# Optimization experiments

Hardware: AMD Instinct MI355X
Metric: run time of the kernel (lower is better)

Reference implementation:

```python
import jax, jax.numpy as jnp
import numpy as np

B, T, C, H = 32, 500, 256, 8  # batch, seq, n_embd(=in_c), heads


def setup_inputs() -> dict:
    key = jax.random.key(0)
    ks = jax.random.split(key, 6)
    s = 0.02
    return {
        "x": jax.random.normal(ks[0], (B, T, C), dtype=jnp.float32),
        # nn.Linear(in_c, 3*n_embd): store as [in, out] for x @ W
        "W_attn": jax.random.normal(ks[1], (C, 3 * C), dtype=jnp.float32) * s,
        "b_attn": jnp.zeros((3 * C,), dtype=jnp.float32),
        # nn.Conv1d(heads, 1, 1, bias=False): a per-head mixing weight [H]
        "p_w": jax.random.normal(ks[2], (H,), dtype=jnp.float32) * s,
        # nn.Linear(n_embd, n_embd)
        "W_proj": jax.random.normal(ks[3], (C, C), dtype=jnp.float32) * s,
        "b_proj": jnp.zeros((C,), dtype=jnp.float32),
    }


def reference(x, W_attn, b_attn, p_w, W_proj, b_proj):
    Bx, Tx, Cx = x.shape
    Hh = p_w.shape[0]
    d = Cx // Hh
    qkv = x @ W_attn + b_attn                          # [B,T,3C]
    q, k, v = jnp.split(qkv, 3, axis=-1)
    # [B,T,C] -> [B,H,T,d]
    q = q.reshape(Bx, Tx, Hh, d).transpose(0, 2, 1, 3)
    k = k.reshape(Bx, Tx, Hh, d).transpose(0, 2, 1, 3)
    v = v.reshape(Bx, Tx, Hh, d).transpose(0, 2, 1, 3)
    scale = 1.0 / np.sqrt(d).astype(np.float32)
    att = jnp.einsum('bhtd,bhsd->bhts', q, k) * scale  # [B,H,T,T]
    # bias buffer is all ones for T<=500, so masked_fill is a no-op
    # pred path: 1x1 conv over heads (weighted sum), then sigmoid
    pred_weight = jax.nn.sigmoid(jnp.einsum('bhts,h->bts', att, p_w))  # [B,T,T]
    pred_weight = jnp.where(jnp.isnan(pred_weight), 0.0, pred_weight)
    # value path: softmax @ V
    a = jax.nn.softmax(att, axis=-1)                   # [B,H,T,T]
    ctx = jnp.einsum('bhts,bhsd->bhtd', a, v)          # [B,H,T,d]
    ctx = ctx.transpose(0, 2, 1, 3).reshape(Bx, Tx, Cx)  # [B,T,C]
    value = ctx @ W_proj + b_proj
    return (pred_weight, value)
```

## Files before the change

### kernel.cpp

```cpp
#include <hip/hip_runtime.h>
#include <stddef.h>

typedef unsigned short u16;
typedef unsigned int u32;
typedef __attribute__((ext_vector_type(4))) float f32x4;
typedef __attribute__((ext_vector_type(8))) u16 u16x8;
typedef __attribute__((ext_vector_type(8))) short s16x8;
typedef __attribute__((ext_vector_type(4))) u32 u32x4;

#define MFMA16 __builtin_amdgcn_mfma_f32_16x16x32_bf16

__device__ __forceinline__ float bf2f(u16 u) { return __uint_as_float(((u32)u) << 16); }
__device__ __forceinline__ u16 f2bf(float f) {
  u32 u = __float_as_uint(f);
  return (u16)((u + 0x7FFFu + ((u >> 16) & 1u)) >> 16);
}
__device__ __forceinline__ u32 cvt_pk_bf16(float lo, float hi) {
  u32 r; asm("v_cvt_pk_bf16_f32 %0, %1, %2" : "=v"(r) : "v"(lo), "v"(hi)); return r;
}

union frag_u { u32x4 u; s16x8 s; };


__global__ __launch_bounds__(256) void gemm_qkv(
    const float* __restrict__ x, const float* __restrict__ W,
    const float* __restrict__ bias, u16* __restrict__ qkbuf, u16* __restrict__ vt)
{
  __shared__ u16 As[128][32];
  __shared__ u16 Bs[64][40];
  const int tid = threadIdx.x;
  const int lane = tid & 63;
  const int w = tid >> 6;
  const int cl = lane & 15, g = lane >> 4;
  const int m0 = blockIdx.x * 128, n0 = blockIdx.y * 64;
  const int wm = w >> 1, wn = w & 1;
  const int bn = tid & 63, bk8 = (tid >> 6) * 8;
  const int ar0 = tid >> 2, ac0 = (tid & 3) * 8;
  const int ar1 = (tid + 256) >> 2, ac1 = ((tid + 256) & 3) * 8;

  f32x4 acc[4][2];
#pragma unroll
  for (int mi = 0; mi < 4; ++mi)
#pragma unroll
    for (int ni = 0; ni < 2; ++ni) acc[mi][ni] = (f32x4){0.f, 0.f, 0.f, 0.f};

  for (int kt = 0; kt < 8; ++kt) {
    const int k0 = kt * 32;
    f32x4 a0l = *(const f32x4*)&x[(size_t)(m0 + ar0) * 256 + k0 + ac0];
    f32x4 a0h = *(const f32x4*)&x[(size_t)(m0 + ar0) * 256 + k0 + ac0 + 4];
    f32x4 a1l = *(const f32x4*)&x[(size_t)(m0 + ar1) * 256 + k0 + ac1];
    f32x4 a1h = *(const f32x4*)&x[(size_t)(m0 + ar1) * 256 + k0 + ac1 + 4];
    float wv[8];
#pragma unroll
    for (int j = 0; j < 8; ++j)
      wv[j] = W[(size_t)(k0 + bk8 + j) * 768 + n0 + bn];
    __syncthreads();
    u32x4 p0, p1;
    p0[0] = cvt_pk_bf16(a0l[0], a0l[1]); p0[1] = cvt_pk_bf16(a0l[2], a0l[3]);
    p0[2] = cvt_pk_bf16(a0h[0], a0h[1]); p0[3] = cvt_pk_bf16(a0h[2], a0h[3]);
    p1[0] = cvt_pk_bf16(a1l[0], a1l[1]); p1[1] = cvt_pk_bf16(a1l[2], a1l[3]);
    p1[2] = cvt_pk_bf16(a1h[0], a1h[1]); p1[3] = cvt_pk_bf16(a1h[2], a1h[3]);
    *(u32x4*)&As[ar0][ac0] = p0;
    *(u32x4*)&As[ar1][ac1] = p1;
    u32x4 bw;
    bw[0] = cvt_pk_bf16(wv[0], wv[1]); bw[1] = cvt_pk_bf16(wv[2], wv[3]);
    bw[2] = cvt_pk_bf16(wv[4], wv[5]); bw[3] = cvt_pk_bf16(wv[6], wv[7]);
    *(u32x4*)&Bs[bn][bk8] = bw;
    __syncthreads();
    s16x8 af[4], bfr[2];
#pragma unroll
    for (int mi = 0; mi < 4; ++mi) af[mi] = *(const s16x8*)&As[wm * 64 + mi * 16 + cl][g * 8];
#pragma unroll
    for (int ni = 0; ni < 2; ++ni) bfr[ni] = *(const s16x8*)&Bs[wn * 32 + ni * 16 + cl][g * 8];
#pragma unroll
    for (int mi = 0; mi < 4; ++mi)
#pragma unroll
      for (int ni = 0; ni < 2; ++ni)
        acc[mi][ni] = MFMA16(af[mi], bfr[ni], acc[mi][ni], 0, 0, 0);
  }
  float bb[2] = { bias[n0 + wn * 32 + cl], bias[n0 + wn * 32 + 16 + cl] };
  if (n0 < 512) {
#pragma unroll
    for (int mi = 0; mi < 4; ++mi)
#pragma unroll
      for (int ni = 0; ni < 2; ++ni)
#pragma unroll
        for (int r = 0; r < 4; ++r) {
          int m = m0 + wm * 64 + mi * 16 + g * 4 + r;
          qkbuf[(size_t)m * 512 + n0 + wn * 32 + ni * 16 + cl] = f2bf(acc[mi][ni][r] + bb[ni]);
        }
  } else {
#pragma unroll
    for (int mi = 0; mi < 4; ++mi)
#pragma unroll
      for (int ni = 0; ni < 2; ++ni) {
        int cb = n0 - 512 + wn * 32 + ni * 16 + cl;
#pragma unroll
        for (int r = 0; r < 4; ++r) {
          int m = m0 + wm * 64 + mi * 16 + g * 4 + r;
          int b2 = m / 500;
          int t2 = m - b2 * 500;
          vt[(size_t)(b2 * 256 + cb) * 500 + t2] = f2bf(acc[mi][ni][r] + bb[ni]);
        }
      }
  }
}

__global__ __launch_bounds__(256) void pred_gemm(
    const u16* __restrict__ qk, const float* __restrict__ pw_g,
    float* __restrict__ pred)
{
  const int tid = threadIdx.x;
  const int lane = tid & 63;
  const int w = tid >> 6;
  const int cl = lane & 15, g = lane >> 4;
  const int lin = blockIdx.x;
  const int xcd = lin & 7, idx = lin >> 3;
  const int b = xcd * 4 + (idx >> 4);
  const int tile = idx & 15;
  const int tm = tile >> 2, tn = tile & 3;
  const int r0 = tm * 128 + (w >> 1) * 64;
  const int c0 = tn * 128 + (w & 1) * 64;
  const float scale = 0.17677669529663687f;

  const u16* qkb = qk + (size_t)b * 500 * 512;
  float fw[8];
#pragma unroll
  for (int h = 0; h < 8; ++h) fw[h] = pw_g[h] * scale;

  f32x4 acc[4][4];
#pragma unroll
  for (int mi = 0; mi < 4; ++mi)
#pragma unroll
    for (int ni = 0; ni < 4; ++ni) acc[mi][ni] = (f32x4){0.f, 0.f, 0.f, 0.f};

#pragma unroll 2
  for (int kt = 0; kt < 8; ++kt) {
    const int k0 = kt * 32;
    s16x8 af[4], bf[4];
#pragma unroll
    for (int mi = 0; mi < 4; ++mi) {
      int t = r0 + mi * 16 + cl; if (t > 499) t = 499;
      af[mi] = *(const s16x8*)&qkb[(size_t)t * 512 + k0 + g * 8];
    }
#pragma unroll
    for (int ni = 0; ni < 4; ++ni) {
      int s = c0 + ni * 16 + cl; if (s > 499) s = 499;
      bf[ni] = *(const s16x8*)&qkb[(size_t)s * 512 + 256 + k0 + g * 8];
    }
    const f32x4 zf = (f32x4){0.f, 0.f, 0.f, 0.f};
    const float f = fw[kt];
#pragma unroll
    for (int mi = 0; mi < 4; ++mi)
#pragma unroll
      for (int ni = 0; ni < 4; ++ni) {
        f32x4 part = MFMA16(af[mi], bf[ni], zf, 0, 0, 0);
#pragma unroll
        for (int r = 0; r < 4; ++r) acc[mi][ni][r] = fmaf(f, part[r], acc[mi][ni][r]);
      }
  }
#pragma unroll
  for (int mi = 0; mi < 4; ++mi)
#pragma unroll
    for (int ni = 0; ni < 4; ++ni) {
      const int s = c0 + ni * 16 + cl;
#pragma unroll
      for (int r = 0; r < 4; ++r) {
        const int t = r0 + mi * 16 + g * 4 + r;
        if (t < 500 && s < 500) {
          pred[(size_t)(b * 500 + t) * 500 + s] =
              1.f / (1.f + __expf(-acc[mi][ni][r]));
        }
      }
    }
}

__global__ __launch_bounds__(256) void attn_value(
    const u16* __restrict__ qk, const u16* __restrict__ vt, u16* __restrict__ ctx)
{
  const int tid = threadIdx.x;
  const int w = tid >> 6;
  const int lane = tid & 63;
  const int cl = lane & 15, g = lane >> 4;
  const int lin = blockIdx.x;
  const int xcd = lin & 7, idx = lin >> 3;
  const int b = xcd * 4 + (idx >> 5);
  const int rem = idx & 31;
  const int h = rem >> 2, qg = rem & 3;
  const int t0 = qg * 128 + w * 32;
  const float scale = 0.17677669529663687f;

  const u16* qkb = qk + (size_t)b * 500 * 512;
  const u16* vtb = vt + (size_t)b * 256 * 500;

  s16x8 qf[2];
#pragma unroll
  for (int qi = 0; qi < 2; ++qi) {
    int tq = t0 + qi * 16 + cl; if (tq > 499) tq = 499;
    qf[qi] = *(const s16x8*)&qkb[(size_t)tq * 512 + h * 32 + g * 8];
  }
  f32x4 of[2][2];
  float lsum[2] = {0.f, 0.f};
#pragma unroll
  for (int qi = 0; qi < 2; ++qi) {
    of[qi][0] = (f32x4){0.f, 0.f, 0.f, 0.f};
    of[qi][1] = (f32x4){0.f, 0.f, 0.f, 0.f};
  }
  const int sA = (g & 1) * 32 + cl;
  const int sB = sA + 16;
  const bool hiHalf = (lane >= 32);

#pragma unroll 1
  for (int st = 0; st < 8; ++st) {
    const int s0 = st * 64;
    s16x8 kf[4];
#pragma unroll
    for (int si = 0; si < 4; ++si) {
      int sr = s0 + si * 16 + cl; if (sr > 499) sr = 499;
      kf[si] = *(const s16x8*)&qkb[(size_t)sr * 512 + 256 + h * 32 + g * 8];
    }
    s16x8 vf[2][2];
#pragma unroll
    for (int di = 0; di < 2; ++di)
#pragma unroll
      for (int s32 = 0; s32 < 2; ++s32)
        vf[di][s32] = *(const s16x8*)&vtb[(size_t)(h * 32 + di * 16 + cl) * 500 +
                                          s0 + s32 * 32 + g * 8];
    const f32x4 zf = (f32x4){0.f, 0.f, 0.f, 0.f};
    u32 P2[2][4][2];
#pragma unroll
    for (int qi = 0; qi < 2; ++qi) {
#pragma unroll
      for (int si = 0; si < 4; ++si) {
        f32x4 St = MFMA16(kf[si], qf[qi], zf, 0, 0, 0);
        float pv[4];
#pragma unroll
        for (int r = 0; r < 4; ++r) {
          int sidx = s0 + si * 16 + g * 4 + r;
          float e = __expf(St[r] * scale);
          pv[r] = (sidx < 500) ? e : 0.f;
          lsum[qi] += pv[r];
        }
        P2[qi][si][0] = cvt_pk_bf16(pv[0], pv[1]);
        P2[qi][si][1] = cvt_pk_bf16(pv[2], pv[3]);
      }
    }
#pragma unroll
    for (int s32 = 0; s32 < 2; ++s32) {
#pragma unroll
      for (int qi = 0; qi < 2; ++qi) {
        u32 Z0 = hiHalf ? P2[qi][2 * s32 + 1][0] : P2[qi][2 * s32][0];
        u32 Z1 = hiHalf ? P2[qi][2 * s32 + 1][1] : P2[qi][2 * s32][1];
        frag_u fu;
        fu.u[0] = (u32)__shfl((int)Z0, sA);
        fu.u[1] = (u32)__shfl((int)Z1, sA);
        fu.u[2] = (u32)__shfl((int)Z0, sB);
        fu.u[3] = (u32)__shfl((int)Z1, sB);
        of[qi][0] = MFMA16(fu.s, vf[0][s32], of[qi][0], 0, 0, 0);
        of[qi][1] = MFMA16(fu.s, vf[1][s32], of[qi][1], 0, 0, 0);
      }
    }
  }
#pragma unroll
  for (int qi = 0; qi < 2; ++qi) {
    float l2 = lsum[qi] + __shfl_xor(lsum[qi], 16);
    l2 += __shfl_xor(l2, 32);
#pragma unroll
    for (int r = 0; r < 4; ++r) {
      const int tq = t0 + qi * 16 + g * 4 + r;
      if (tq < 500) {
        const float inv = 1.f / __shfl(l2, g * 4 + r);
        ctx[(size_t)(b * 500 + tq) * 256 + h * 32 + cl]      = f2bf(of[qi][0][r] * inv);
        ctx[(size_t)(b * 500 + tq) * 256 + h * 32 + 16 + cl] = f2bf(of[qi][1][r] * inv);
      }
    }
  }
}

__global__ __launch_bounds__(256) void gemm_proj(
    const u16* __restrict__ A, const float* __restrict__ W,
    const float* __restrict__ bias, float* __restrict__ out)
{
  __shared__ u16 As[128][32];
  __shared__ u16 Bs[64][40];
  const int tid = threadIdx.x;
  const int lane = tid & 63;
  const int w = tid >> 6;
  const int cl = lane & 15, g = lane >> 4;
  const int m0 = blockIdx.x * 128, n0 = blockIdx.y * 64;
  const int wm = w >> 1, wn = w & 1;
  const int bn = tid & 63, bk8 = (tid >> 6) * 8;
  const int ar0 = tid >> 2, ac0 = (tid & 3) * 8;
  const int ar1 = (tid + 256) >> 2, ac1 = ((tid + 256) & 3) * 8;

  f32x4 acc[4][2];
#pragma unroll
  for (int mi = 0; mi < 4; ++mi)
#pragma unroll
    for (int ni = 0; ni < 2; ++ni) acc[mi][ni] = (f32x4){0.f, 0.f, 0.f, 0.f};

  for (int kt = 0; kt < 8; ++kt) {
    const int k0 = kt * 32;
    u16x8 a0 = *(const u16x8*)&A[(size_t)(m0 + ar0) * 256 + k0 + ac0];
    u16x8 a1 = *(const u16x8*)&A[(size_t)(m0 + ar1) * 256 + k0 + ac1];
    float wv[8];
#pragma unroll
    for (int j = 0; j < 8; ++j)
      wv[j] = W[(size_t)(k0 + bk8 + j) * 256 + n0 + bn];
    __syncthreads();
    *(u16x8*)&As[ar0][ac0] = a0;
    *(u16x8*)&As[ar1][ac1] = a1;
    u32x4 bw;
    bw[0] = cvt_pk_bf16(wv[0], wv[1]); bw[1] = cvt_pk_bf16(wv[2], wv[3]);
    bw[2] = cvt_pk_bf16(wv[4], wv[5]); bw[3] = cvt_pk_bf16(wv[6], wv[7]);
    *(u32x4*)&Bs[bn][bk8] = bw;
    __syncthreads();
    s16x8 af[4], bfr[2];
#pragma unroll
    for (int mi = 0; mi < 4; ++mi) af[mi] = *(const s16x8*)&As[wm * 64 + mi * 16 + cl][g * 8];
#pragma unroll
    for (int ni = 0; ni < 2; ++ni) bfr[ni] = *(const s16x8*)&Bs[wn * 32 + ni * 16 + cl][g * 8];
#pragma unroll
    for (int mi = 0; mi < 4; ++mi)
#pragma unroll
      for (int ni = 0; ni < 2; ++ni)
        acc[mi][ni] = MFMA16(af[mi], bfr[ni], acc[mi][ni], 0, 0, 0);
  }
  float bb[2] = { bias[n0 + wn * 32 + cl], bias[n0 + wn * 32 + 16 + cl] };
#pragma unroll
  for (int mi = 0; mi < 4; ++mi)
#pragma unroll
    for (int ni = 0; ni < 2; ++ni)
#pragma unroll
      for (int r = 0; r < 4; ++r) {
        int m = m0 + wm * 64 + mi * 16 + g * 4 + r;
        out[(size_t)m * 256 + n0 + wn * 32 + ni * 16 + cl] = acc[mi][ni][r] + bb[ni];
      }
}

extern "C" void kernel_launch(void* const* d_in, const int* in_sizes, int n_in,
                              void* d_out, int out_size, void* d_ws, size_t ws_size,
                              hipStream_t stream)
{
  const float* x      = (const float*)d_in[0];
  const float* W_attn = (const float*)d_in[1];
  const float* b_attn = (const float*)d_in[2];
  const float* p_w    = (const float*)d_in[3];
  const float* W_proj = (const float*)d_in[4];
  const float* b_proj = (const float*)d_in[5];

  float* pred   = (float*)d_out;
  float* valout = pred + 8000000;

  u16* qkbuf = (u16*)d_ws;
  u16* vt    = (u16*)((char*)d_ws + 16384000);
  u16* ctx   = (u16*)((char*)d_ws + 24576000);

  hipLaunchKernelGGL(gemm_qkv, dim3(125, 12), dim3(256), 0, stream,
                     x, W_attn, b_attn, qkbuf, vt);
  hipLaunchKernelGGL(pred_gemm, dim3(512), dim3(256), 0, stream,
                     qkbuf, p_w, pred);
  hipLaunchKernelGGL(attn_value, dim3(1024), dim3(256), 0, stream,
                     qkbuf, vt, ctx);
  hipLaunchKernelGGL(gemm_proj, dim3(125, 4), dim3(256), 0, stream,
                     ctx, W_proj, b_proj, valout);
}
```

Baseline: 104.3 us.

## Pre-transpose weights to bf16 and restructure QKV/proj GEMMs with full-K A tiles

```diff
diff --git a/kernel.cpp b/kernel.cpp
--- a/kernel.cpp
+++ b/kernel.cpp
@@ -5,7 +5,9 @@
 typedef unsigned int u32;
 typedef __attribute__((ext_vector_type(4))) float f32x4;
 typedef __attribute__((ext_vector_type(8))) u16 u16x8;
+typedef __attribute__((ext_vector_type(4))) u16 u16x4;
 typedef __attribute__((ext_vector_type(8))) short s16x8;
+typedef __attribute__((ext_vector_type(2))) u32 u32x2;
 typedef __attribute__((ext_vector_type(4))) u32 u32x4;
 
 #define MFMA16 __builtin_amdgcn_mfma_f32_16x16x32_bf16
@@ -22,87 +24,114 @@
 union frag_u { u32x4 u; s16x8 s; };
 
 
-__global__ __launch_bounds__(256) void gemm_qkv(
-    const float* __restrict__ x, const float* __restrict__ W,
+__global__ __launch_bounds__(256) void transpose_w(
+    const float* __restrict__ W, u16* __restrict__ Wt, int K, int N)
+{
+  __shared__ u16 T[64][72];
+  const int tid = threadIdx.x;
+  const int k0 = blockIdx.x * 64, n0 = blockIdx.y * 64;
+#pragma unroll
+  for (int it = 0; it < 4; ++it) {
+    const int r = it * 16 + (tid >> 4);
+    const int c = (tid & 15) * 4;
+    f32x4 v = *(const f32x4*)&W[(size_t)(k0 + r) * N + n0 + c];
+    u16x4 o;
+    o[0] = f2bf(v[0]); o[1] = f2bf(v[1]); o[2] = f2bf(v[2]); o[3] = f2bf(v[3]);
+    *(u16x4*)&T[r][c] = o;
+  }
+  __syncthreads();
+#pragma unroll
+  for (int it = 0; it < 4; ++it) {
+    const int n = it * 16 + (tid >> 4);
+    const int kc = (tid & 15) * 4;
+    u16x4 o;
+    o[0] = T[kc + 0][n]; o[1] = T[kc + 1][n];
+    o[2] = T[kc + 2][n]; o[3] = T[kc + 3][n];
+    *(u16x4*)&Wt[(size_t)(n0 + n) * K + k0 + kc] = o;
+  }
+}
+
+__global__ __launch_bounds__(512, 2) void gemm_qkv(
+    const float* __restrict__ x, const u16* __restrict__ WtA,
     const float* __restrict__ bias, u16* __restrict__ qkbuf, u16* __restrict__ vt)
 {
-  __shared__ u16 As[128][32];
-  __shared__ u16 Bs[64][40];
+  __shared__ u16 As[64][264];
   const int tid = threadIdx.x;
   const int lane = tid & 63;
   const int w = tid >> 6;
   const int cl = lane & 15, g = lane >> 4;
-  const int m0 = blockIdx.x * 128, n0 = blockIdx.y * 64;
-  const int wm = w >> 1, wn = w & 1;
-  const int bn = tid & 63, bk8 = (tid >> 6) * 8;
-  const int ar0 = tid >> 2, ac0 = (tid & 3) * 8;
-  const int ar1 = (tid + 256) >> 2, ac1 = ((tid + 256) & 3) * 8;
-
-  f32x4 acc[4][2];
-#pragma unroll
-  for (int mi = 0; mi < 4; ++mi)
-#pragma unroll
-    for (int ni = 0; ni < 2; ++ni) acc[mi][ni] = (f32x4){0.f, 0.f, 0.f, 0.f};
-
-  for (int kt = 0; kt < 8; ++kt) {
-    const int k0 = kt * 32;
-    f32x4 a0l = *(const f32x4*)&x[(size_t)(m0 + ar0) * 256 + k0 + ac0];
-    f32x4 a0h = *(const f32x4*)&x[(size_t)(m0 + ar0) * 256 + k0 + ac0 + 4];
-    f32x4 a1l = *(const f32x4*)&x[(size_t)(m0 + ar1) * 256 + k0 + ac1];
-    f32x4 a1h = *(const f32x4*)&x[(size_t)(m0 + ar1) * 256 + k0 + ac1 + 4];
-    float wv[8];
-#pragma unroll
-    for (int j = 0; j < 8; ++j)
-      wv[j] = W[(size_t)(k0 + bk8 + j) * 768 + n0 + bn];
-    __syncthreads();
-    u32x4 p0, p1;
-    p0[0] = cvt_pk_bf16(a0l[0], a0l[1]); p0[1] = cvt_pk_bf16(a0l[2], a0l[3]);
-    p0[2] = cvt_pk_bf16(a0h[0], a0h[1]); p0[3] = cvt_pk_bf16(a0h[2], a0h[3]);
-    p1[0] = cvt_pk_bf16(a1l[0], a1l[1]); p1[1] = cvt_pk_bf16(a1l[2], a1l[3]);
-    p1[2] = cvt_pk_bf16(a1h[0], a1h[1]); p1[3] = cvt_pk_bf16(a1h[2], a1h[3]);
-    *(u32x4*)&As[ar0][ac0] = p0;
-    *(u32x4*)&As[ar1][ac1] = p1;
-    u32x4 bw;
-    bw[0] = cvt_pk_bf16(wv[0], wv[1]); bw[1] = cvt_pk_bf16(wv[2], wv[3]);
-    bw[2] = cvt_pk_bf16(wv[4], wv[5]); bw[3] = cvt_pk_bf16(wv[6], wv[7]);
-    *(u32x4*)&Bs[bn][bk8] = bw;
-    __syncthreads();
-    s16x8 af[4], bfr[2];
-#pragma unroll
-    for (int mi = 0; mi < 4; ++mi) af[mi] = *(const s16x8*)&As[wm * 64 + mi * 16 + cl][g * 8];
-#pragma unroll
-    for (int ni = 0; ni < 2; ++ni) bfr[ni] = *(const s16x8*)&Bs[wn * 32 + ni * 16 + cl][g * 8];
-#pragma unroll
-    for (int mi = 0; mi < 4; ++mi)
-#pragma unroll
-      for (int ni = 0; ni < 2; ++ni)
-        acc[mi][ni] = MFMA16(af[mi], bfr[ni], acc[mi][ni], 0, 0, 0);
-  }
-  float bb[2] = { bias[n0 + wn * 32 + cl], bias[n0 + wn * 32 + 16 + cl] };
-  if (n0 < 512) {
-#pragma unroll
-    for (int mi = 0; mi < 4; ++mi)
-#pragma unroll
-      for (int ni = 0; ni < 2; ++ni)
-#pragma unroll
-        for (int r = 0; r < 4; ++r) {
-          int m = m0 + wm * 64 + mi * 16 + g * 4 + r;
-          qkbuf[(size_t)m * 512 + n0 + wn * 32 + ni * 16 + cl] = f2bf(acc[mi][ni][r] + bb[ni]);
+  const int wm = w >> 2, wn = w & 3;
+  const int m0 = blockIdx.x * 64;
+
+#pragma unroll
+  for (int it = 0; it < 4; ++it) {
+    const int ci = tid + it * 512;
+    const int row = ci >> 5;
+    const int c8 = (ci & 31) * 8;
+    f32x4 lo = *(const f32x4*)&x[(size_t)(m0 + row) * 256 + c8];
+    f32x4 hi = *(const f32x4*)&x[(size_t)(m0 + row) * 256 + c8 + 4];
+    u32x4 p;
+    p[0] = cvt_pk_bf16(lo[0], lo[1]); p[1] = cvt_pk_bf16(lo[2], lo[3]);
+    p[2] = cvt_pk_bf16(hi[0], hi[1]); p[3] = cvt_pk_bf16(hi[2], hi[3]);
+    *(u32x4*)&As[row][c8] = p;
+  }
+  __syncthreads();
+
+  s16x8 af[2][8];
+#pragma unroll
+  for (int mi = 0; mi < 2; ++mi)
+#pragma unroll
+    for (int kt = 0; kt < 8; ++kt)
+      af[mi][kt] = *(const s16x8*)&As[wm * 32 + mi * 16 + cl][kt * 32 + g * 8];
+
+#pragma unroll 1
+  for (int nc = 0; nc < 3; ++nc) {
+    const int n0 = wn * 192 + nc * 64;
+    f32x4 acc[2][4];
+#pragma unroll
+    for (int mi = 0; mi < 2; ++mi)
+#pragma unroll
+      for (int ni = 0; ni < 4; ++ni) acc[mi][ni] = (f32x4){0.f, 0.f, 0.f, 0.f};
+#pragma unroll
+    for (int kt = 0; kt < 8; ++kt) {
+      s16x8 bf[4];
+#pragma unroll
+      for (int ni = 0; ni < 4; ++ni)
+        bf[ni] = *(const s16x8*)&WtA[(size_t)(n0 + ni * 16 + cl) * 256 + kt * 32 + g * 8];
+#pragma unroll
+      for (int mi = 0; mi < 2; ++mi)
+#pragma unroll
+        for (int ni = 0; ni < 4; ++ni)
+          acc[mi][ni] = MFMA16(af[mi][kt], bf[ni], acc[mi][ni], 0, 0, 0);
+    }
+    float bb[4];
+#pragma unroll
+    for (int ni = 0; ni < 4; ++ni) bb[ni] = bias[n0 + ni * 16 + cl];
+    if (n0 < 512) {
+#pragma unroll
+      for (int mi = 0; mi < 2; ++mi)
+#pragma unroll
+        for (int ni = 0; ni < 4; ++ni)
+#pragma unroll
+          for (int r = 0; r < 4; ++r) {
+            const int m = m0 + wm * 32 + mi * 16 + g * 4 + r;
+            qkbuf[(size_t)m * 512 + n0 + ni * 16 + cl] = f2bf(acc[mi][ni][r] + bb[ni]);
+          }
+    } else {
+#pragma unroll
+      for (int mi = 0; mi < 2; ++mi)
+#pragma unroll
+        for (int ni = 0; ni < 4; ++ni) {
+          const int cb = n0 - 512 + ni * 16 + cl;
+#pragma unroll
+          for (int r = 0; r < 4; ++r) {
+            const int m = m0 + wm * 32 + mi * 16 + g * 4 + r;
+            const int b2 = m / 500;
+            const int t2 = m - b2 * 500;
+            vt[(size_t)(b2 * 256 + cb) * 500 + t2] = f2bf(acc[mi][ni][r] + bb[ni]);
+          }
         }
-  } else {
-#pragma unroll
-    for (int mi = 0; mi < 4; ++mi)
-#pragma unroll
-      for (int ni = 0; ni < 2; ++ni) {
-        int cb = n0 - 512 + wn * 32 + ni * 16 + cl;
-#pragma unroll
-        for (int r = 0; r < 4; ++r) {
-          int m = m0 + wm * 64 + mi * 16 + g * 4 + r;
-          int b2 = m / 500;
-          int t2 = m - b2 * 500;
-          vt[(size_t)(b2 * 256 + cb) * 500 + t2] = f2bf(acc[mi][ni][r] + bb[ni]);
-        }
-      }
+    }
   }
 }
 
@@ -277,64 +306,63 @@
   }
 }
 
-__global__ __launch_bounds__(256) void gemm_proj(
-    const u16* __restrict__ A, const float* __restrict__ W,
+__global__ __launch_bounds__(512, 2) void gemm_proj(
+    const u16* __restrict__ ctx, const u16* __restrict__ WtP,
     const float* __restrict__ bias, float* __restrict__ out)
 {
-  __shared__ u16 As[128][32];
-  __shared__ u16 Bs[64][40];
+  __shared__ u16 As[64][264];
   const int tid = threadIdx.x;
   const int lane = tid & 63;
   const int w = tid >> 6;
   const int cl = lane & 15, g = lane >> 4;
-  const int m0 = blockIdx.x * 128, n0 = blockIdx.y * 64;
-  const int wm = w >> 1, wn = w & 1;
-  const int bn = tid & 63, bk8 = (tid >> 6) * 8;
-  const int ar0 = tid >> 2, ac0 = (tid & 3) * 8;
-  const int ar1 = (tid + 256) >> 2, ac1 = ((tid + 256) & 3) * 8;
-
-  f32x4 acc[4][2];
-#pragma unroll
-  for (int mi = 0; mi < 4; ++mi)
-#pragma unroll
-    for (int ni = 0; ni < 2; ++ni) acc[mi][ni] = (f32x4){0.f, 0.f, 0.f, 0.f};
-
+  const int wm = w >> 2, wn = w & 3;
+  const int m0 = blockIdx.x * 64;
+
+#pragma unroll
+  for (int it = 0; it < 4; ++it) {
+    const int ci = tid + it * 512;
+    const int row = ci >> 5;
+    const int c8 = (ci & 31) * 8;
+    *(u32x4*)&As[row][c8] = *(const u32x4*)&ctx[(size_t)(m0 + row) * 256 + c8];
+  }
+  __syncthreads();
+
+  s16x8 af[2][8];
+#pragma unroll
+  for (int mi = 0; mi < 2; ++mi)
+#pragma unroll
+    for (int kt = 0; kt < 8; ++kt)
+      af[mi][kt] = *(const s16x8*)&As[wm * 32 + mi * 16 + cl][kt * 32 + g * 8];
+
+  const int n0 = wn * 64;
+  f32x4 acc[2][4];
+#pragma unroll
+  for (int mi = 0; mi < 2; ++mi)
+#pragma unroll
+    for (int ni = 0; ni < 4; ++ni) acc[mi][ni] = (f32x4){0.f, 0.f, 0.f, 0.f};
+#pragma unroll
   for (int kt = 0; kt < 8; ++kt) {
-    const int k0 = kt * 32;
-    u16x8 a0 = *(const u16x8*)&A[(size_t)(m0 + ar0) * 256 + k0 + ac0];
-    u16x8 a1 = *(const u16x8*)&A[(size_t)(m0 + ar1) * 256 + k0 + ac1];
-    float wv[8];
-#pragma unroll
-    for (int j = 0; j < 8; ++j)
-      wv[j] = W[(size_t)(k0 + bk8 + j) * 256 + n0 + bn];
-    __syncthreads();
-    *(u16x8*)&As[ar0][ac0] = a0;
-    *(u16x8*)&As[ar1][ac1] = a1;
-    u32x4 bw;
-    bw[0] = cvt_pk_bf16(wv[0], wv[1]); bw[1] = cvt_pk_bf16(wv[2], wv[3]);
-    bw[2] = cvt_pk_bf16(wv[4], wv[5]); bw[3] = cvt_pk_bf16(wv[6], wv[7]);
-    *(u32x4*)&Bs[bn][bk8] = bw;
-    __syncthreads();
-    s16x8 af[4], bfr[2];
-#pragma unroll
-    for (int mi = 0; mi < 4; ++mi) af[mi] = *(const s16x8*)&As[wm * 64 + mi * 16 + cl][g * 8];
-#pragma unroll
-    for (int ni = 0; ni < 2; ++ni) bfr[ni] = *(const s16x8*)&Bs[wn * 32 + ni * 16 + cl][g * 8];
-#pragma unroll
-    for (int mi = 0; mi < 4; ++mi)
-#pragma unroll
-      for (int ni = 0; ni < 2; ++ni)
-        acc[mi][ni] = MFMA16(af[mi], bfr[ni], acc[mi][ni], 0, 0, 0);
-  }
-  float bb[2] = { bias[n0 + wn * 32 + cl], bias[n0 + wn * 32 + 16 + cl] };
-#pragma unroll
-  for (int mi = 0; mi < 4; ++mi)
-#pragma unroll
-    for (int ni = 0; ni < 2; ++ni)
+    s16x8 bf[4];
+#pragma unroll
+    for (int ni = 0; ni < 4; ++ni)
+      bf[ni] = *(const s16x8*)&WtP[(size_t)(n0 + ni * 16 + cl) * 256 + kt * 32 + g * 8];
+#pragma unroll
+    for (int mi = 0; mi < 2; ++mi)
+#pragma unroll
+      for (int ni = 0; ni < 4; ++ni)
+        acc[mi][ni] = MFMA16(af[mi][kt], bf[ni], acc[mi][ni], 0, 0, 0);
+  }
+  float bb[4];
+#pragma unroll
+  for (int ni = 0; ni < 4; ++ni) bb[ni] = bias[n0 + ni * 16 + cl];
+#pragma unroll
+  for (int mi = 0; mi < 2; ++mi)
+#pragma unroll
+    for (int ni = 0; ni < 4; ++ni)
 #pragma unroll
       for (int r = 0; r < 4; ++r) {
-        int m = m0 + wm * 64 + mi * 16 + g * 4 + r;
-        out[(size_t)m * 256 + n0 + wn * 32 + ni * 16 + cl] = acc[mi][ni][r] + bb[ni];
+        const int m = m0 + wm * 32 + mi * 16 + g * 4 + r;
+        out[(size_t)m * 256 + n0 + ni * 16 + cl] = acc[mi][ni][r] + bb[ni];
       }
 }
 
@@ -355,13 +383,19 @@
   u16* qkbuf = (u16*)d_ws;
   u16* vt    = (u16*)((char*)d_ws + 16384000);
   u16* ctx   = (u16*)((char*)d_ws + 24576000);
-
-  hipLaunchKernelGGL(gemm_qkv, dim3(125, 12), dim3(256), 0, stream,
-                     x, W_attn, b_attn, qkbuf, vt);
+  u16* WtA   = ctx;
+  u16* WtP   = qkbuf;
+
+  hipLaunchKernelGGL(transpose_w, dim3(4, 12), dim3(256), 0, stream,
+                     W_attn, WtA, 256, 768);
+  hipLaunchKernelGGL(gemm_qkv, dim3(250), dim3(512), 0, stream,
+                     x, WtA, b_attn, qkbuf, vt);
   hipLaunchKernelGGL(pred_gemm, dim3(512), dim3(256), 0, stream,
                      qkbuf, p_w, pred);
   hipLaunchKernelGGL(attn_value, dim3(1024), dim3(256), 0, stream,
                      qkbuf, vt, ctx);
-  hipLaunchKernelGGL(gemm_proj, dim3(125, 4), dim3(256), 0, stream,
-                     ctx, W_proj, b_proj, valout);
-}
+  hipLaunchKernelGGL(transpose_w, dim3(4, 4), dim3(256), 0, stream,
+                     W_proj, WtP, 256, 256);
+  hipLaunchKernelGGL(gemm_proj, dim3(250), dim3(512), 0, stream,
+                     ctx, WtP, b_proj, valout);
+}
```

Result: slower. 107.0 us (+2.5%).
